# Kernel tuning notes

Measured on AMD Instinct MI355X. Metric: run time of the kernel, lower is better.

Reference implementation:

```python
import jax, jax.numpy as jnp
import numpy as np

H, NH, NKV, HD, I = 4096, 32, 8, 128, 14336
B, S = 1, 2048
THETA = 500000.0
EPS = 1e-5
SCALE = HD ** -0.5


def setup_inputs() -> dict:
    key = jax.random.key(0)
    ks = jax.random.split(key, 8)
    sc = 0.02
    return {
        "positions": jnp.arange(S, dtype=jnp.int32),
        "hidden_states": jax.random.normal(ks[0], (B, S, H), jnp.float32),
        "residual": jax.random.normal(ks[1], (B, S, H), jnp.float32),
        "w_qkv": jax.random.normal(ks[2], ((NH + 2 * NKV) * HD, H), jnp.float32) * sc,
        "w_o": jax.random.normal(ks[3], (H, NH * HD), jnp.float32) * sc,
        "w_gate_up": jax.random.normal(ks[4], (2 * I, H), jnp.float32) * sc,
        "w_down": jax.random.normal(ks[5], (H, I), jnp.float32) * sc,
        "w_ln1": jnp.ones((H,), jnp.float32),
        "w_ln2": jnp.ones((H,), jnp.float32),
    }


def rmsnorm(x, w):
    xf = x.astype(jnp.float32)
    y = xf * jax.lax.rsqrt(jnp.mean(xf * xf, axis=-1, keepdims=True) + EPS)
    return (y * w).astype(x.dtype)


def apply_rope(x, positions):
    # x: [B, S, nh, HD]; neox style: rotate halves
    half = HD // 2
    inv_freq = 1.0 / (THETA ** (jnp.arange(0, half, dtype=jnp.float32) / half))
    freqs = positions.astype(jnp.float32)[:, None] * inv_freq[None, :]  # [S, half]
    cos = jnp.cos(freqs)[None, :, None, :]
    sin = jnp.sin(freqs)[None, :, None, :]
    x1, x2 = x[..., :half], x[..., half:]
    return jnp.concatenate([x1 * cos - x2 * sin, x2 * cos + x1 * sin], axis=-1)


def reference(positions, hidden_states, residual, w_qkv, w_o, w_gate_up, w_down, w_ln1, w_ln2):
    # fused add + RMSNorm (input_layernorm with residual)
    residual = hidden_states + residual
    h = rmsnorm(residual, w_ln1)

    # fused QKV projection
    qkv = jnp.einsum('bsh,oh->bso', h, w_qkv)
    q = qkv[..., : NH * HD].reshape(B, S, NH, HD)
    k = qkv[..., NH * HD: (NH + NKV) * HD].reshape(B, S, NKV, HD)
    v = qkv[..., (NH + NKV) * HD:].reshape(B, S, NKV, HD)

    q = apply_rope(q, positions)
    k = apply_rope(k, positions)

    # GQA: expand kv heads
    rep = NH // NKV
    k = jnp.repeat(k, rep, axis=2)  # [B,S,NH,HD]
    v = jnp.repeat(v, rep, axis=2)

    scores = jnp.einsum('bqhd,bkhd->bhqk', q, k) * SCALE
    causal = jnp.tril(jnp.ones((S, S), bool))
    scores = jnp.where(causal[None, None], scores, jnp.float32(-1e30))
    attn = jax.nn.softmax(scores, axis=-1)
    ctx = jnp.einsum('bhqk,bkhd->bqhd', attn, v).reshape(B, S, NH * HD)
    attn_out = jnp.einsum('bso,ho->bsh', ctx, w_o)

    # fused add + RMSNorm (post_attention_layernorm)
    residual = attn_out + residual
    h = rmsnorm(residual, w_ln2)

    # SwiGLU MLP
    gu = jnp.einsum('bsh,oh->bso', h, w_gate_up)
    gate, up = gu[..., :I], gu[..., I:]
    h = jax.nn.silu(gate) * up
    out = jnp.einsum('bsi,hi->bsh', h, w_down)
    return out, residual
```

## Files before the change

kernel.cpp:

```cpp
#include <hip/hip_runtime.h>

typedef short bf16x8 __attribute__((ext_vector_type(8)));
typedef short short4v __attribute__((ext_vector_type(4)));
typedef float f32x4 __attribute__((ext_vector_type(4)));

#define SCALE_ATTN 0.08838834764831845f

__device__ inline short f2bs(float f) {
    unsigned u = __builtin_bit_cast(unsigned, f);
    unsigned r = (u + 0x7fffu + ((u >> 16) & 1u)) >> 16;
    return (short)(unsigned short)r;
}
__device__ inline float b2f(short s) {
    unsigned u = ((unsigned)(unsigned short)s) << 16;
    return __builtin_bit_cast(float, u);
}
__device__ inline void pack_w(const float4& a, const float4& b, bf16x8& p) {
    p[0] = f2bs(a.x); p[1] = f2bs(a.y); p[2] = f2bs(a.z); p[3] = f2bs(a.w);
    p[4] = f2bs(b.x); p[5] = f2bs(b.y); p[6] = f2bs(b.z); p[7] = f2bs(b.w);
}

__global__ __launch_bounds__(256)
void wconv_kernel(const float* __restrict__ src, short* __restrict__ dst, long n8)
{
    const long stride = (long)gridDim.x << 8;
    for (long i = ((long)blockIdx.x << 8) + threadIdx.x; i < n8; i += stride) {
        const float4 a = ((const float4*)src)[i << 1];
        const float4 b = ((const float4*)src)[(i << 1) + 1];
        bf16x8 p;
        pack_w(a, b, p);
        ((bf16x8*)dst)[i] = p;
    }
}

__global__ __launch_bounds__(256)
void add_rmsnorm_kernel(const float* __restrict__ X, const float* __restrict__ Rin,
                        const float* __restrict__ w, float* __restrict__ Rout,
                        short* __restrict__ Hout)
{
    const int tid = threadIdx.x;
    const long base = (long)blockIdx.x << 12;
    float v[16];
    float ss = 0.f;
#pragma unroll
    for (int p = 0; p < 4; ++p) {
        const int idx = (p << 10) + (tid << 2);
        float4 a = *(const float4*)(X + base + idx);
        if (Rin != nullptr) {
            float4 b = *(const float4*)(Rin + base + idx);
            a.x += b.x; a.y += b.y; a.z += b.z; a.w += b.w;
        }
        v[p*4+0] = a.x; v[p*4+1] = a.y; v[p*4+2] = a.z; v[p*4+3] = a.w;
        ss += a.x*a.x + a.y*a.y + a.z*a.z + a.w*a.w;
    }
#pragma unroll
    for (int dd = 1; dd < 64; dd <<= 1) ss += __shfl_xor(ss, dd);
    __shared__ float red[4];
    if ((tid & 63) == 0) red[tid >> 6] = ss;
    __syncthreads();
    const float tot = red[0] + red[1] + red[2] + red[3];
    const float rstd = rsqrtf(tot * (1.0f / 4096.0f) + 1e-5f);
#pragma unroll
    for (int p = 0; p < 4; ++p) {
        const int idx = (p << 10) + (tid << 2);
        if (Rout != nullptr) {
            float4 b; b.x = v[p*4+0]; b.y = v[p*4+1]; b.z = v[p*4+2]; b.w = v[p*4+3];
            *(float4*)(Rout + base + idx) = b;
        }
        float4 wv4 = *(const float4*)(w + idx);
        short4v hb;
        hb[0] = f2bs(v[p*4+0] * rstd * wv4.x);
        hb[1] = f2bs(v[p*4+1] * rstd * wv4.y);
        hb[2] = f2bs(v[p*4+2] * rstd * wv4.z);
        hb[3] = f2bs(v[p*4+3] * rstd * wv4.w);
        *(short4v*)(Hout + base + idx) = hb;
    }
}

#define BAR()   do { asm volatile("" ::: "memory"); __builtin_amdgcn_s_barrier(); asm volatile("" ::: "memory"); } while (0)
#define LGKM0() asm volatile("s_waitcnt lgkmcnt(0)" ::: "memory")
#define VMW(n)  asm volatile("s_waitcnt vmcnt(" #n ")" ::: "memory")

__device__ inline bf16x8 lds_frag(const short* tile, int row, int kb) {
    const int off = row * 128 + (kb ^ ((row & 7) << 4));
    return *(const bf16x8*)((const char*)tile + off);
}

__device__ inline void stage_half(const short* __restrict__ G, long grow0, long K,
                                  long k0, short* ldsHalf, int wv, int lane)
{
#pragma unroll
    for (int i = 0; i < 2; ++i) {
        short* dst = ldsHalf + ((i << 13) + (wv << 10)) / 2;
        const int off = (wv << 10) + (i << 13) + (lane << 4);
        const int r   = off >> 7;
        const int cb  = off & 127;
        const int gcb = cb ^ ((r & 7) << 4);
        const short* src = G + (grow0 + r) * K + k0 + (gcb >> 1);
        __builtin_amdgcn_global_load_lds(
            (const __attribute__((address_space(1))) void*)(const void*)src,
            (__attribute__((address_space(3))) void*)(void*)dst, 16, 0, 0);
    }
}

#define LOAD_A(T, grp) do {                                        \
    _Pragma("unroll") for (int _m = 0; _m < 4; ++_m) {             \
        const int _row = abase + (grp)*64 + _m*16 + l15;           \
        a[_m][0] = lds_frag(T, _row, l4b);                         \
        a[_m][1] = lds_frag(T, _row, 64 + l4b);                    \
    } } while (0)

#define LOAD_B(T, n0) do {                                         \
    _Pragma("unroll") for (int _n = 0; _n < 2; ++_n) {             \
        const int _row = bbase + ((n0)+_n)*16 + l15;               \
        b[(n0)+_n][0] = lds_frag(T, _row, l4b);                    \
        b[(n0)+_n][1] = lds_frag(T, _row, 64 + l4b);               \
    } } while (0)

#define MFMA16(MB, NB) do {                                                        \
    __builtin_amdgcn_s_setprio(1);                                                 \
    _Pragma("unroll") for (int _m = 0; _m < 4; ++_m)                               \
    _Pragma("unroll") for (int _n = 0; _n < 2; ++_n) {                             \
        acc[(MB)+_m][(NB)+_n] = __builtin_amdgcn_mfma_f32_16x16x32_bf16(           \
            a[_m][0], b[(NB)+_n][0], acc[(MB)+_m][(NB)+_n], 0, 0, 0);              \
        acc[(MB)+_m][(NB)+_n] = __builtin_amdgcn_mfma_f32_16x16x32_bf16(           \
            a[_m][1], b[(NB)+_n][1], acc[(MB)+_m][(NB)+_n], 0, 0, 0);              \
    }                                                                              \
    __builtin_amdgcn_s_setprio(0);                                                 \
} while (0)

template<int EPI>
__global__ __launch_bounds__(512, 2)
void gemm8(const short* __restrict__ A, const short* __restrict__ W,
           float* __restrict__ Cf, short* __restrict__ Cb,
           const float* __restrict__ resid, int N, int K)
{
    __shared__ __align__(16) short As[2][16384];
    __shared__ __align__(16) short Bs[2][16384];

    const int tid  = threadIdx.x;
    const int lane = tid & 63;
    const int wv   = tid >> 6;
    const int wm   = wv >> 2;
    const int wn   = wv & 3;
    const int l15  = lane & 15;
    const int l4b  = (lane >> 4) << 4;

    const int nwg  = gridDim.x << 3;
    const int cpx  = nwg >> 3;
    const int orig = (blockIdx.y * gridDim.x) + blockIdx.x;
    const int lgc  = (orig & 7) * cpx + (orig >> 3);
    const int bx   = lgc >> 3;
    const int by   = lgc & 7;

    const long row0 = (long)by << 8;
    const long col0 = (long)bx << 8;
    const int abase = wm << 7;
    const int bbase = wn << 6;

    f32x4 acc[8][4];
#pragma unroll
    for (int i = 0; i < 8; ++i)
#pragma unroll
        for (int j = 0; j < 4; ++j) acc[i][j] = (f32x4){0.f,0.f,0.f,0.f};

    bf16x8 a[4][2], b[4][2];
    const int iters = K >> 7;

    stage_half(A, row0,       K, 0,  &As[0][0],    wv, lane);
    stage_half(A, row0 + 128, K, 0,  &As[0][8192], wv, lane);
    stage_half(W, col0,       K, 0,  &Bs[0][0],    wv, lane);
    stage_half(W, col0 + 128, K, 0,  &Bs[0][8192], wv, lane);
    stage_half(A, row0,       K, 64, &As[1][0],    wv, lane);
    stage_half(A, row0 + 128, K, 64, &As[1][8192], wv, lane);
    stage_half(W, col0,       K, 64, &Bs[1][0],    wv, lane);
    stage_half(W, col0 + 128, K, 64, &Bs[1][8192], wv, lane);
    VMW(8);
    BAR();

#pragma unroll 1
    for (int it = 0; it < iters; ++it) {
        const long k2 = ((long)(2*it + 2)) << 6;
        const long k3 = k2 + 64;
        const bool pf = (it + 1 < iters);

        LOAD_A(As[0], 0); LOAD_B(Bs[0], 0);
        BAR(); LGKM0(); MFMA16(0, 0); BAR();
        LOAD_B(Bs[0], 2);
        BAR(); LGKM0(); MFMA16(0, 2); BAR();
        LOAD_A(As[0], 1);
        if (pf) stage_half(W, col0, K, k2, &Bs[0][0], wv, lane);
        BAR(); LGKM0(); MFMA16(4, 0); BAR();
        if (pf) {
            stage_half(A, row0,       K, k2, &As[0][0],    wv, lane);
            stage_half(W, col0 + 128, K, k2, &Bs[0][8192], wv, lane);
        }
        VMW(6);
        BAR(); MFMA16(4, 2); BAR();

        LOAD_A(As[1], 0); LOAD_B(Bs[1], 0);
        if (pf) stage_half(A, row0 + 128, K, k2, &As[0][8192], wv, lane);
        BAR(); LGKM0(); MFMA16(0, 0); BAR();
        LOAD_B(Bs[1], 2);
        BAR(); LGKM0(); MFMA16(0, 2); BAR();
        LOAD_A(As[1], 1);
        if (pf) {
            stage_half(W, col0,       K, k3, &Bs[1][0],    wv, lane);
            stage_half(W, col0 + 128, K, k3, &Bs[1][8192], wv, lane);
        }
        BAR(); LGKM0(); MFMA16(4, 0); BAR();
        if (pf) {
            stage_half(A, row0,       K, k3, &As[1][0],    wv, lane);
            stage_half(A, row0 + 128, K, k3, &As[1][8192], wv, lane);
        }
        VMW(8);
        BAR(); MFMA16(4, 2); BAR();
    }

#pragma unroll
    for (int m = 0; m < 8; ++m) {
#pragma unroll
        for (int n = 0; n < 4; ++n) {
            const long gr = row0 + (wm << 7) + m*16 + ((lane >> 4) << 2);
            const long gc = col0 + (wn << 6) + n*16 + l15;
#pragma unroll
            for (int r = 0; r < 4; ++r) {
                const float v = acc[m][n][r];
                const long idx = (gr + r) * N + gc;
                if (EPI == 0)      Cf[idx] = v;
                else if (EPI == 1) Cf[idx] = v + resid[idx];
                else               Cb[idx] = f2bs(v);
            }
        }
    }
}

__global__ __launch_bounds__(128)
void rope_kernel(const int* __restrict__ pos, const float* __restrict__ qkv,
                 short* __restrict__ Qo, short* __restrict__ Ko)
{
    const int h = blockIdx.x;
    const int s = blockIdx.y;
    const int d = threadIdx.x;
    const int j = d & 63;
    const float p = (float)pos[s];
    const float invf = __expf((float)j * -0.20503692895f);
    float sn, cs;
    __sincosf(p * invf, &sn, &cs);
    const long base = (long)s * 6144 + h * 128;
    const float x1 = qkv[base + j];
    const float x2 = qkv[base + 64 + j];
    const float outv = (d < 64) ? (x1 * cs - x2 * sn) : (x2 * cs + x1 * sn);
    const short ob = f2bs(outv);
    if (h < 32) Qo[(long)s * 4096 + h * 128 + d] = ob;
    else        Ko[(long)s * 1024 + (h - 32) * 128 + d] = ob;
}

__global__ __launch_bounds__(256)
void vtrans_kernel(const float* __restrict__ qkv, short* __restrict__ Vt)
{
    __shared__ short tile[64][136];
    const int tid = threadIdx.x;
    const int s0 = blockIdx.x << 6;
    const int h = blockIdx.y;
    {
        const int srow = tid >> 2;
        const int c0 = (tid & 3) << 5;
        const float* src = qkv + (long)(s0 + srow) * 6144 + 5120 + h * 128 + c0;
#pragma unroll
        for (int m = 0; m < 8; ++m) {
            float4 f = *(const float4*)(src + (m << 2));
            tile[srow][c0 + (m << 2) + 0] = f2bs(f.x);
            tile[srow][c0 + (m << 2) + 1] = f2bs(f.y);
            tile[srow][c0 + (m << 2) + 2] = f2bs(f.z);
            tile[srow][c0 + (m << 2) + 3] = f2bs(f.w);
        }
    }
    __syncthreads();
    {
        const int d = tid >> 1;
        const int sc = (tid & 1) << 5;
        short* dst = Vt + ((long)h * 128 + d) * 2048 + s0 + sc;
#pragma unroll
        for (int m = 0; m < 4; ++m) {
            bf16x8 v;
#pragma unroll
            for (int e = 0; e < 8; ++e) v[e] = tile[sc + (m << 3) + e][d];
            *(bf16x8*)(dst + (m << 3)) = v;
        }
    }
}

__global__ __launch_bounds__(256)
void flash_kernel(const short* __restrict__ Qg, const short* __restrict__ Kg,
                  const short* __restrict__ Vtg, short* __restrict__ Ctx)
{
    __shared__ short Qs[64 * 128];
    __shared__ short Ks[64 * 128];
    __shared__ short Vs[128 * 64];
    __shared__ short Ps[4 * 16 * 64];

    const int tid  = threadIdx.x;
    const int lane = tid & 63;
    const int wv   = tid >> 6;
    const int l15  = lane & 15;
    const int l4e  = (lane >> 4) << 3;
    const int qt   = blockIdx.x;
    const int head = blockIdx.y;
    const int q0   = qt << 6;
    const int kvh  = head >> 2;

    {
        const int row = tid >> 2;
        const int c0 = (tid & 3) << 5;
        const short* src = Qg + (long)(q0 + row) * 4096 + head * 128 + c0;
        const int sw = (row & 7) << 3;
#pragma unroll
        for (int m = 0; m < 4; ++m) {
            bf16x8 v = *(const bf16x8*)(src + (m << 3));
            *(bf16x8*)&Qs[row * 128 + ((c0 + (m << 3)) ^ sw)] = v;
        }
    }

    float mrow[4], lrow[4];
    f32x4 o[8];
#pragma unroll
    for (int r = 0; r < 4; ++r) { mrow[r] = -__builtin_inff(); lrow[r] = 0.f; }
#pragma unroll
    for (int d = 0; d < 8; ++d) o[d] = (f32x4){0.f,0.f,0.f,0.f};

    for (int t = 0; t <= qt; ++t) {
        const int kv0 = t << 6;
        __syncthreads();
        {
            const int row = tid >> 2;
            const int c0 = (tid & 3) << 5;
            const short* src = Kg + (long)(kv0 + row) * 1024 + kvh * 128 + c0;
            const int sw = (row & 7) << 3;
#pragma unroll
            for (int m = 0; m < 4; ++m) {
                bf16x8 v = *(const bf16x8*)(src + (m << 3));
                *(bf16x8*)&Ks[row * 128 + ((c0 + (m << 3)) ^ sw)] = v;
            }
        }
        {
            const int d = tid >> 1;
            const int c0 = (tid & 1) << 5;
            const short* src = Vtg + ((long)kvh * 128 + d) * 2048 + kv0 + c0;
            const int sw = (d & 7) << 3;
#pragma unroll
            for (int m = 0; m < 4; ++m) {
                bf16x8 v = *(const bf16x8*)(src + (m << 3));
                *(bf16x8*)&Vs[d * 64 + ((c0 + (m << 3)) ^ sw)] = v;
            }
        }
        __syncthreads();

        bf16x8 qa[4];
        {
            const int qrow = (wv << 4) + l15;
            const int sw = (qrow & 7) << 3;
#pragma unroll
            for (int kk = 0; kk < 4; ++kk)
                qa[kk] = *(const bf16x8*)&Qs[qrow * 128 + ((l4e + (kk << 5)) ^ sw)];
        }
        f32x4 sacc[4];
#pragma unroll
        for (int j = 0; j < 4; ++j) {
            sacc[j] = (f32x4){0.f,0.f,0.f,0.f};
            const int krow = (j << 4) + l15;
            const int sw = (krow & 7) << 3;
#pragma unroll
            for (int kk = 0; kk < 4; ++kk) {
                bf16x8 kb8 = *(const bf16x8*)&Ks[krow * 128 + ((l4e + (kk << 5)) ^ sw)];
                sacc[j] = __builtin_amdgcn_mfma_f32_16x16x32_bf16(qa[kk], kb8, sacc[j], 0, 0, 0);
            }
        }

#pragma unroll
        for (int ri = 0; ri < 4; ++ri) {
            const int grow = q0 + (wv << 4) + ((lane >> 4) << 2) + ri;
            float sv[4];
#pragma unroll
            for (int j = 0; j < 4; ++j) {
                float s = sacc[j][ri] * SCALE_ATTN;
                const int col = kv0 + (j << 4) + l15;
                sv[j] = (col > grow) ? -1e30f : s;
            }
            float mx = fmaxf(fmaxf(sv[0], sv[1]), fmaxf(sv[2], sv[3]));
#pragma unroll
            for (int dd = 1; dd < 16; dd <<= 1) mx = fmaxf(mx, __shfl_xor(mx, dd));
            const float mnew = fmaxf(mrow[ri], mx);
            const float alpha = __expf(mrow[ri] - mnew);
            mrow[ri] = mnew;
            float psum = 0.f;
            short pb[4];
#pragma unroll
            for (int j = 0; j < 4; ++j) {
                float p = __expf(sv[j] - mnew);
                psum += p;
                pb[j] = f2bs(p);
            }
            lrow[ri] = lrow[ri] * alpha + psum;
#pragma unroll
            for (int d = 0; d < 8; ++d) o[d][ri] *= alpha;
            const int prow = ((lane >> 4) << 2) + ri;
            const int sw = (prow & 7) << 3;
#pragma unroll
            for (int j = 0; j < 4; ++j)
                Ps[(wv << 10) + prow * 64 + ((((j << 4) + l15)) ^ sw)] = pb[j];
        }

        bf16x8 pa0, pa1;
        {
            const int prow = l15;
            const int sw = (prow & 7) << 3;
            pa0 = *(const bf16x8*)&Ps[(wv << 10) + prow * 64 + (l4e ^ sw)];
            pa1 = *(const bf16x8*)&Ps[(wv << 10) + prow * 64 + ((l4e + 32) ^ sw)];
        }
#pragma unroll
        for (int fd = 0; fd < 8; ++fd) {
            const int drow = (fd << 4) + l15;
            const int sw = (drow & 7) << 3;
            bf16x8 v0 = *(const bf16x8*)&Vs[drow * 64 + (l4e ^ sw)];
            bf16x8 v1 = *(const bf16x8*)&Vs[drow * 64 + ((l4e + 32) ^ sw)];
            o[fd] = __builtin_amdgcn_mfma_f32_16x16x32_bf16(pa0, v0, o[fd], 0, 0, 0);
            o[fd] = __builtin_amdgcn_mfma_f32_16x16x32_bf16(pa1, v1, o[fd], 0, 0, 0);
        }
    }

    float inv[4];
#pragma unroll
    for (int ri = 0; ri < 4; ++ri) {
        float ls = lrow[ri];
#pragma unroll
        for (int dd = 1; dd < 16; dd <<= 1) ls += __shfl_xor(ls, dd);
        inv[ri] = 1.0f / ls;
    }
#pragma unroll
    for (int fd = 0; fd < 8; ++fd)
#pragma unroll
        for (int ri = 0; ri < 4; ++ri) {
            const long row = q0 + (wv << 4) + ((lane >> 4) << 2) + ri;
            Ctx[row * 4096 + head * 128 + (fd << 4) + l15] = f2bs(o[fd][ri] * inv[ri]);
        }
}

__global__ __launch_bounds__(256)
void silu_kernel(const short* __restrict__ gu, short* __restrict__ hm)
{
    const int s = blockIdx.y;
    const int j = ((blockIdx.x << 8) + threadIdx.x) << 3;
    const short* g = gu + (long)s * 28672 + j;
    bf16x8 gv = *(const bf16x8*)g;
    bf16x8 uv = *(const bf16x8*)(g + 14336);
    bf16x8 ov;
#pragma unroll
    for (int e = 0; e < 8; ++e) {
        const float gf = b2f(gv[e]);
        const float uf = b2f(uv[e]);
        const float r = gf / (1.f + __expf(-gf)) * uf;
        ov[e] = f2bs(r);
    }
    *(bf16x8*)(hm + (long)s * 14336 + j) = ov;
}

extern "C" void kernel_launch(void* const* d_in, const int* in_sizes, int n_in,
                              void* d_out, int out_size, void* d_ws, size_t ws_size,
                              hipStream_t stream)
{
    const int*   positions = (const int*)d_in[0];
    const float* hidden    = (const float*)d_in[1];
    const float* residual  = (const float*)d_in[2];
    const float* w_qkv     = (const float*)d_in[3];
    const float* w_o       = (const float*)d_in[4];
    const float* w_gu      = (const float*)d_in[5];
    const float* w_down    = (const float*)d_in[6];
    const float* w_ln1     = (const float*)d_in[7];
    const float* w_ln2     = (const float*)d_in[8];

    float* out_f   = (float*)d_out;
    float* resid2  = out_f + 8388608;
    float* resid1  = out_f;

    char* wsb = (char*)d_ws;
    short* h1     = (short*)(wsb + 0);
    short* ctx    = (short*)(wsb + 0);
    float* qkvbuf = (float*)(wsb + 16777216);
    short* h2     = (short*)(wsb + 16777216);
    short* qb     = (short*)(wsb + 67108864);
    short* kb     = (short*)(wsb + 83886080);
    short* vt     = (short*)(wsb + 88080384);
    short* gu     = (short*)(wsb + 33554432);
    short* hm     = (short*)(wsb + 150994944);
    short* wbuf   = (short*)(wsb + 209715200);

    add_rmsnorm_kernel<<<2048, 256, 0, stream>>>(hidden, residual, w_ln1, resid1, h1);
    wconv_kernel<<<2048, 256, 0, stream>>>(w_qkv, wbuf, 3145728L);
    gemm8<0><<<dim3(24, 8), 512, 0, stream>>>(h1, wbuf, qkvbuf, nullptr, nullptr, 6144, 4096);
    rope_kernel<<<dim3(40, 2048), 128, 0, stream>>>(positions, qkvbuf, qb, kb);
    vtrans_kernel<<<dim3(32, 8), 256, 0, stream>>>(qkvbuf, vt);
    flash_kernel<<<dim3(32, 32), 256, 0, stream>>>(qb, kb, vt, ctx);
    wconv_kernel<<<2048, 256, 0, stream>>>(w_o, wbuf, 2097152L);
    gemm8<1><<<dim3(16, 8), 512, 0, stream>>>(ctx, wbuf, resid2, nullptr, resid1, 4096, 4096);
    add_rmsnorm_kernel<<<2048, 256, 0, stream>>>(resid2, nullptr, w_ln2, nullptr, h2);
    wconv_kernel<<<2048, 256, 0, stream>>>(w_gu, wbuf, 14680064L);
    gemm8<2><<<dim3(112, 8), 512, 0, stream>>>(h2, wbuf, nullptr, gu, nullptr, 28672, 4096);
    silu_kernel<<<dim3(7, 2048), 256, 0, stream>>>(gu, hm);
    wconv_kernel<<<2048, 256, 0, stream>>>(w_down, wbuf, 7340032L);
    gemm8<0><<<dim3(16, 8), 512, 0, stream>>>(hm, wbuf, out_f, nullptr, nullptr, 4096, 14336);
}
```

Measured before the change: 1.578 ms.

## Add split-K to small-N GEMMs and register double-buffer LDS fragments

Adds a KS template parameter so the O-projection and down-projection GEMMs split K in two across a third grid dimension. This doubles the workgroup count from 128 to 256 so more CUs are busy. The partial sums go to fp32 workspace and are reduced in the following add+rmsnorm kernel or a new add2 kernel. Separately, the GEMM main loop now double-buffers A/B fragments in registers (Aa/Ab, B0/B1) and drops the explicit lgkmcnt waits, so LDS reads overlap with MFMAs. The cost is extra fp32 partial traffic and higher register pressure.

```diff
diff --git a/kernel.cpp b/kernel.cpp
--- a/kernel.cpp
+++ b/kernel.cpp
@@ -34,9 +34,9 @@
 }
 
 __global__ __launch_bounds__(256)
-void add_rmsnorm_kernel(const float* __restrict__ X, const float* __restrict__ Rin,
-                        const float* __restrict__ w, float* __restrict__ Rout,
-                        short* __restrict__ Hout)
+void add_rmsnorm_kernel(const float* __restrict__ X, const float* __restrict__ X2,
+                        const float* __restrict__ Rin, const float* __restrict__ w,
+                        float* __restrict__ Rout, short* __restrict__ Hout)
 {
     const int tid = threadIdx.x;
     const long base = (long)blockIdx.x << 12;
@@ -46,6 +46,10 @@
     for (int p = 0; p < 4; ++p) {
         const int idx = (p << 10) + (tid << 2);
         float4 a = *(const float4*)(X + base + idx);
+        if (X2 != nullptr) {
+            float4 b = *(const float4*)(X2 + base + idx);
+            a.x += b.x; a.y += b.y; a.z += b.z; a.w += b.w;
+        }
         if (Rin != nullptr) {
             float4 b = *(const float4*)(Rin + base + idx);
             a.x += b.x; a.y += b.y; a.z += b.z; a.w += b.w;
@@ -77,8 +81,20 @@
     }
 }
 
+__global__ __launch_bounds__(256)
+void add2_kernel(const float* __restrict__ a, const float* __restrict__ b,
+                 float* __restrict__ o, long n4)
+{
+    const long st = (long)gridDim.x << 8;
+    for (long i = ((long)blockIdx.x << 8) + threadIdx.x; i < n4; i += st) {
+        float4 x = ((const float4*)a)[i];
+        float4 y = ((const float4*)b)[i];
+        x.x += y.x; x.y += y.y; x.z += y.z; x.w += y.w;
+        ((float4*)o)[i] = x;
+    }
+}
+
 #define BAR()   do { asm volatile("" ::: "memory"); __builtin_amdgcn_s_barrier(); asm volatile("" ::: "memory"); } while (0)
-#define LGKM0() asm volatile("s_waitcnt lgkmcnt(0)" ::: "memory")
 #define VMW(n)  asm volatile("s_waitcnt vmcnt(" #n ")" ::: "memory")
 
 __device__ inline bf16x8 lds_frag(const short* tile, int row, int kb) {
@@ -103,33 +119,33 @@
     }
 }
 
-#define LOAD_A(T, grp) do {                                        \
+#define LOADA_(dst, T, grp) do {                                   \
     _Pragma("unroll") for (int _m = 0; _m < 4; ++_m) {             \
         const int _row = abase + (grp)*64 + _m*16 + l15;           \
-        a[_m][0] = lds_frag(T, _row, l4b);                         \
-        a[_m][1] = lds_frag(T, _row, 64 + l4b);                    \
+        dst[_m][0] = lds_frag(T, _row, l4b);                       \
+        dst[_m][1] = lds_frag(T, _row, 64 + l4b);                  \
     } } while (0)
 
-#define LOAD_B(T, n0) do {                                         \
+#define LOADB_(dst, T, n0) do {                                    \
     _Pragma("unroll") for (int _n = 0; _n < 2; ++_n) {             \
         const int _row = bbase + ((n0)+_n)*16 + l15;               \
-        b[(n0)+_n][0] = lds_frag(T, _row, l4b);                    \
-        b[(n0)+_n][1] = lds_frag(T, _row, 64 + l4b);               \
+        dst[_n][0] = lds_frag(T, _row, l4b);                       \
+        dst[_n][1] = lds_frag(T, _row, 64 + l4b);                  \
     } } while (0)
 
-#define MFMA16(MB, NB) do {                                                        \
+#define MFMA16_(AR, BR, MB, NB) do {                                               \
     __builtin_amdgcn_s_setprio(1);                                                 \
     _Pragma("unroll") for (int _m = 0; _m < 4; ++_m)                               \
     _Pragma("unroll") for (int _n = 0; _n < 2; ++_n) {                             \
         acc[(MB)+_m][(NB)+_n] = __builtin_amdgcn_mfma_f32_16x16x32_bf16(           \
-            a[_m][0], b[(NB)+_n][0], acc[(MB)+_m][(NB)+_n], 0, 0, 0);              \
+            AR[_m][0], BR[_n][0], acc[(MB)+_m][(NB)+_n], 0, 0, 0);                 \
         acc[(MB)+_m][(NB)+_n] = __builtin_amdgcn_mfma_f32_16x16x32_bf16(           \
-            a[_m][1], b[(NB)+_n][1], acc[(MB)+_m][(NB)+_n], 0, 0, 0);              \
+            AR[_m][1], BR[_n][1], acc[(MB)+_m][(NB)+_n], 0, 0, 0);                 \
     }                                                                              \
     __builtin_amdgcn_s_setprio(0);                                                 \
 } while (0)
 
-template<int EPI>
+template<int EPI, int KS>
 __global__ __launch_bounds__(512, 2)
 void gemm8(const short* __restrict__ A, const short* __restrict__ W,
            float* __restrict__ Cf, short* __restrict__ Cb,
@@ -146,77 +162,99 @@
     const int l15  = lane & 15;
     const int l4b  = (lane >> 4) << 4;
 
-    const int nwg  = gridDim.x << 3;
+    const int gx   = gridDim.x;
+    const int nwg  = gx * 8 * KS;
     const int cpx  = nwg >> 3;
-    const int orig = (blockIdx.y * gridDim.x) + blockIdx.x;
+    const int orig = (blockIdx.z * 8 + blockIdx.y) * gx + blockIdx.x;
     const int lgc  = (orig & 7) * cpx + (orig >> 3);
-    const int bx   = lgc >> 3;
     const int by   = lgc & 7;
+    const int tq   = lgc >> 3;
+    const int kz   = (KS == 1) ? 0 : (tq % KS);
+    const int bx   = (KS == 1) ? tq : (tq / KS);
 
     const long row0 = (long)by << 8;
     const long col0 = (long)bx << 8;
     const int abase = wm << 7;
     const int bbase = wn << 6;
 
+    const int  Kc    = K / KS;
+    const long kbase = (long)kz * Kc;
+    const int  iters = Kc >> 7;
+
     f32x4 acc[8][4];
 #pragma unroll
     for (int i = 0; i < 8; ++i)
 #pragma unroll
         for (int j = 0; j < 4; ++j) acc[i][j] = (f32x4){0.f,0.f,0.f,0.f};
 
-    bf16x8 a[4][2], b[4][2];
-    const int iters = K >> 7;
-
-    stage_half(A, row0,       K, 0,  &As[0][0],    wv, lane);
-    stage_half(A, row0 + 128, K, 0,  &As[0][8192], wv, lane);
-    stage_half(W, col0,       K, 0,  &Bs[0][0],    wv, lane);
-    stage_half(W, col0 + 128, K, 0,  &Bs[0][8192], wv, lane);
-    stage_half(A, row0,       K, 64, &As[1][0],    wv, lane);
-    stage_half(A, row0 + 128, K, 64, &As[1][8192], wv, lane);
-    stage_half(W, col0,       K, 64, &Bs[1][0],    wv, lane);
-    stage_half(W, col0 + 128, K, 64, &Bs[1][8192], wv, lane);
+    bf16x8 Aa[4][2], Ab[4][2], B0[2][2], B1[2][2];
+
+    stage_half(A, row0,       K, kbase,      &As[0][0],    wv, lane);
+    stage_half(A, row0 + 128, K, kbase,      &As[0][8192], wv, lane);
+    stage_half(W, col0,       K, kbase,      &Bs[0][0],    wv, lane);
+    stage_half(W, col0 + 128, K, kbase,      &Bs[0][8192], wv, lane);
+    stage_half(A, row0,       K, kbase + 64, &As[1][0],    wv, lane);
+    stage_half(A, row0 + 128, K, kbase + 64, &As[1][8192], wv, lane);
+    stage_half(W, col0,       K, kbase + 64, &Bs[1][0],    wv, lane);
+    stage_half(W, col0 + 128, K, kbase + 64, &Bs[1][8192], wv, lane);
     VMW(8);
     BAR();
+    LOADA_(Aa, As[0], 0); LOADB_(B0, Bs[0], 0);
 
 #pragma unroll 1
     for (int it = 0; it < iters; ++it) {
-        const long k2 = ((long)(2*it + 2)) << 6;
+        const long k2 = kbase + ((long)(2*it + 2) << 6);
         const long k3 = k2 + 64;
         const bool pf = (it + 1 < iters);
 
-        LOAD_A(As[0], 0); LOAD_B(Bs[0], 0);
-        BAR(); LGKM0(); MFMA16(0, 0); BAR();
-        LOAD_B(Bs[0], 2);
-        BAR(); LGKM0(); MFMA16(0, 2); BAR();
-        LOAD_A(As[0], 1);
+        BAR();
+        LOADB_(B1, Bs[0], 2);
+        MFMA16_(Aa, B0, 0, 0);
+        BAR();
+        LOADA_(Ab, As[0], 1);
+        MFMA16_(Aa, B1, 0, 2);
+        BAR();
         if (pf) stage_half(W, col0, K, k2, &Bs[0][0], wv, lane);
-        BAR(); LGKM0(); MFMA16(4, 0); BAR();
+        BAR();
+        MFMA16_(Ab, B0, 4, 0);
+        BAR();
         if (pf) {
             stage_half(A, row0,       K, k2, &As[0][0],    wv, lane);
             stage_half(W, col0 + 128, K, k2, &Bs[0][8192], wv, lane);
         }
         VMW(6);
-        BAR(); MFMA16(4, 2); BAR();
-
-        LOAD_A(As[1], 0); LOAD_B(Bs[1], 0);
+        BAR();
+        LOADA_(Aa, As[1], 0); LOADB_(B0, Bs[1], 0);
+        MFMA16_(Ab, B1, 4, 2);
+        BAR();
         if (pf) stage_half(A, row0 + 128, K, k2, &As[0][8192], wv, lane);
-        BAR(); LGKM0(); MFMA16(0, 0); BAR();
-        LOAD_B(Bs[1], 2);
-        BAR(); LGKM0(); MFMA16(0, 2); BAR();
-        LOAD_A(As[1], 1);
+        BAR();
+        LOADB_(B1, Bs[1], 2);
+        MFMA16_(Aa, B0, 0, 0);
+        BAR();
+        LOADA_(Ab, As[1], 1);
+        MFMA16_(Aa, B1, 0, 2);
+        BAR();
         if (pf) {
             stage_half(W, col0,       K, k3, &Bs[1][0],    wv, lane);
             stage_half(W, col0 + 128, K, k3, &Bs[1][8192], wv, lane);
         }
-        BAR(); LGKM0(); MFMA16(4, 0); BAR();
+        BAR();
+        MFMA16_(Ab, B0, 4, 0);
+        BAR();
         if (pf) {
             stage_half(A, row0,       K, k3, &As[1][0],    wv, lane);
             stage_half(A, row0 + 128, K, k3, &As[1][8192], wv, lane);
         }
         VMW(8);
-        BAR(); MFMA16(4, 2); BAR();
-    }
-
+        BAR();
+        if (pf) { LOADA_(Aa, As[0], 0); LOADB_(B0, Bs[0], 0); }
+        MFMA16_(Ab, B1, 4, 2);
+        BAR();
+    }
+
+    float* Cfp = Cf;
+    if (KS > 1) Cfp = Cf + (long)kz * ((long)N << 11);
 #pragma unroll
     for (int m = 0; m < 8; ++m) {
 #pragma unroll
@@ -227,8 +265,8 @@
             for (int r = 0; r < 4; ++r) {
                 const float v = acc[m][n][r];
                 const long idx = (gr + r) * N + gc;
-                if (EPI == 0)      Cf[idx] = v;
-                else if (EPI == 1) Cf[idx] = v + resid[idx];
+                if (EPI == 0)      Cfp[idx] = v;
+                else if (EPI == 1) Cfp[idx] = v + resid[idx];
                 else               Cb[idx] = f2bs(v);
             }
         }
@@ -491,22 +529,25 @@
     short* qb     = (short*)(wsb + 67108864);
     short* kb     = (short*)(wsb + 83886080);
     short* vt     = (short*)(wsb + 88080384);
+    float* Po     = (float*)(wsb + 100663296);
     short* gu     = (short*)(wsb + 33554432);
     short* hm     = (short*)(wsb + 150994944);
+    float* Pd     = (float*)(wsb + 0);
     short* wbuf   = (short*)(wsb + 209715200);
 
-    add_rmsnorm_kernel<<<2048, 256, 0, stream>>>(hidden, residual, w_ln1, resid1, h1);
+    add_rmsnorm_kernel<<<2048, 256, 0, stream>>>(hidden, nullptr, residual, w_ln1, resid1, h1);
     wconv_kernel<<<2048, 256, 0, stream>>>(w_qkv, wbuf, 3145728L);
-    gemm8<0><<<dim3(24, 8), 512, 0, stream>>>(h1, wbuf, qkvbuf, nullptr, nullptr, 6144, 4096);
+    gemm8<0,1><<<dim3(24, 8, 1), 512, 0, stream>>>(h1, wbuf, qkvbuf, nullptr, nullptr, 6144, 4096);
     rope_kernel<<<dim3(40, 2048), 128, 0, stream>>>(positions, qkvbuf, qb, kb);
     vtrans_kernel<<<dim3(32, 8), 256, 0, stream>>>(qkvbuf, vt);
     flash_kernel<<<dim3(32, 32), 256, 0, stream>>>(qb, kb, vt, ctx);
     wconv_kernel<<<2048, 256, 0, stream>>>(w_o, wbuf, 2097152L);
-    gemm8<1><<<dim3(16, 8), 512, 0, stream>>>(ctx, wbuf, resid2, nullptr, resid1, 4096, 4096);
-    add_rmsnorm_kernel<<<2048, 256, 0, stream>>>(resid2, nullptr, w_ln2, nullptr, h2);
+    gemm8<0,2><<<dim3(16, 8, 2), 512, 0, stream>>>(ctx, wbuf, Po, nullptr, nullptr, 4096, 4096);
+    add_rmsnorm_kernel<<<2048, 256, 0, stream>>>(Po, Po + 8388608, resid1, w_ln2, resid2, h2);
     wconv_kernel<<<2048, 256, 0, stream>>>(w_gu, wbuf, 14680064L);
-    gemm8<2><<<dim3(112, 8), 512, 0, stream>>>(h2, wbuf, nullptr, gu, nullptr, 28672, 4096);
+    gemm8<2,1><<<dim3(112, 8, 1), 512, 0, stream>>>(h2, wbuf, nullptr, gu, nullptr, 28672, 4096);
     silu_kernel<<<dim3(7, 2048), 256, 0, stream>>>(gu, hm);
     wconv_kernel<<<2048, 256, 0, stream>>>(w_down, wbuf, 7340032L);
-    gemm8<0><<<dim3(16, 8), 512, 0, stream>>>(hm, wbuf, out_f, nullptr, nullptr, 4096, 14336);
-}
+    gemm8<0,2><<<dim3(16, 8, 2), 512, 0, stream>>>(hm, wbuf, Pd, nullptr, nullptr, 4096, 14336);
+    add2_kernel<<<2048, 256, 0, stream>>>(Pd, Pd + 8388608, out_f, 2097152L);
+}
```

Result: slower. 1.775 ms (+12.5%).

## Split-K for O/down GEMMs and fuse SiLU into gate-up GEMM epilogue

Applied to the files above, without the earlier changes.

Adds a split-K template parameter to the GEMM so the O-projection and down-projection grids run two K-halves into partial buffers. The partials are summed in the following add+RMSNorm kernel and in a new add kernel. The gate/up weights are interleaved in 128-row tiles during conversion so each output tile holds matching gate and up columns. SiLU is then applied in the GEMM epilogue through LDS, which removes the separate SiLU kernel and the bf16 gate-up round trip. The cost is extra partial-sum traffic in fp32 and one more small kernel for the down projection.

```diff
diff --git a/kernel.cpp b/kernel.cpp
--- a/kernel.cpp
+++ b/kernel.cpp
@@ -33,10 +33,25 @@
     }
 }
 
+__global__ __launch_bounds__(512)
+void wconv_gu_kernel(const float* __restrict__ src, short* __restrict__ dst)
+{
+    const int n = blockIdx.x;
+    const int t = n >> 8, r = n & 255;
+    const int orig = (r < 128) ? (t * 128 + r) : (14336 + t * 128 + (r - 128));
+    const float* s = src + (long)orig * 4096;
+    short* d = dst + (long)n * 4096;
+    const int j = threadIdx.x << 3;
+    float4 a = *(const float4*)(s + j);
+    float4 b = *(const float4*)(s + j + 4);
+    bf16x8 p; pack_w(a, b, p);
+    *(bf16x8*)(d + j) = p;
+}
+
 __global__ __launch_bounds__(256)
-void add_rmsnorm_kernel(const float* __restrict__ X, const float* __restrict__ Rin,
-                        const float* __restrict__ w, float* __restrict__ Rout,
-                        short* __restrict__ Hout)
+void add_rmsnorm_kernel(const float* __restrict__ X, const float* __restrict__ X2,
+                        const float* __restrict__ Rin, const float* __restrict__ w,
+                        float* __restrict__ Rout, short* __restrict__ Hout)
 {
     const int tid = threadIdx.x;
     const long base = (long)blockIdx.x << 12;
@@ -46,6 +61,10 @@
     for (int p = 0; p < 4; ++p) {
         const int idx = (p << 10) + (tid << 2);
         float4 a = *(const float4*)(X + base + idx);
+        if (X2 != nullptr) {
+            float4 b = *(const float4*)(X2 + base + idx);
+            a.x += b.x; a.y += b.y; a.z += b.z; a.w += b.w;
+        }
         if (Rin != nullptr) {
             float4 b = *(const float4*)(Rin + base + idx);
             a.x += b.x; a.y += b.y; a.z += b.z; a.w += b.w;
@@ -74,6 +93,19 @@
         hb[2] = f2bs(v[p*4+2] * rstd * wv4.z);
         hb[3] = f2bs(v[p*4+3] * rstd * wv4.w);
         *(short4v*)(Hout + base + idx) = hb;
+    }
+}
+
+__global__ __launch_bounds__(256)
+void add2_kernel(const float* __restrict__ a, const float* __restrict__ b,
+                 float* __restrict__ o, long n4)
+{
+    const long st = (long)gridDim.x << 8;
+    for (long i = ((long)blockIdx.x << 8) + threadIdx.x; i < n4; i += st) {
+        float4 x = ((const float4*)a)[i];
+        float4 y = ((const float4*)b)[i];
+        x.x += y.x; x.y += y.y; x.z += y.z; x.w += y.w;
+        ((float4*)o)[i] = x;
     }
 }
 
@@ -129,11 +161,11 @@
     __builtin_amdgcn_s_setprio(0);                                                 \
 } while (0)
 
-template<int EPI>
+template<int EPI, int KS>
 __global__ __launch_bounds__(512, 2)
 void gemm8(const short* __restrict__ A, const short* __restrict__ W,
            float* __restrict__ Cf, short* __restrict__ Cb,
-           const float* __restrict__ resid, int N, int K)
+           int N, int K)
 {
     __shared__ __align__(16) short As[2][16384];
     __shared__ __align__(16) short Bs[2][16384];
@@ -146,18 +178,25 @@
     const int l15  = lane & 15;
     const int l4b  = (lane >> 4) << 4;
 
-    const int nwg  = gridDim.x << 3;
+    const int gx   = gridDim.x;
+    const int nwg  = gx * 8 * KS;
     const int cpx  = nwg >> 3;
-    const int orig = (blockIdx.y * gridDim.x) + blockIdx.x;
+    const int orig = (blockIdx.z * 8 + blockIdx.y) * gx + blockIdx.x;
     const int lgc  = (orig & 7) * cpx + (orig >> 3);
-    const int bx   = lgc >> 3;
     const int by   = lgc & 7;
+    const int tq   = lgc >> 3;
+    const int kz   = (KS == 1) ? 0 : (tq % KS);
+    const int bx   = (KS == 1) ? tq : (tq / KS);
 
     const long row0 = (long)by << 8;
     const long col0 = (long)bx << 8;
     const int abase = wm << 7;
     const int bbase = wn << 6;
 
+    const int  Kc    = K / KS;
+    const long kbase = (long)kz * Kc;
+    const int  iters = Kc >> 7;
+
     f32x4 acc[8][4];
 #pragma unroll
     for (int i = 0; i < 8; ++i)
@@ -165,22 +204,21 @@
         for (int j = 0; j < 4; ++j) acc[i][j] = (f32x4){0.f,0.f,0.f,0.f};
 
     bf16x8 a[4][2], b[4][2];
-    const int iters = K >> 7;
-
-    stage_half(A, row0,       K, 0,  &As[0][0],    wv, lane);
-    stage_half(A, row0 + 128, K, 0,  &As[0][8192], wv, lane);
-    stage_half(W, col0,       K, 0,  &Bs[0][0],    wv, lane);
-    stage_half(W, col0 + 128, K, 0,  &Bs[0][8192], wv, lane);
-    stage_half(A, row0,       K, 64, &As[1][0],    wv, lane);
-    stage_half(A, row0 + 128, K, 64, &As[1][8192], wv, lane);
-    stage_half(W, col0,       K, 64, &Bs[1][0],    wv, lane);
-    stage_half(W, col0 + 128, K, 64, &Bs[1][8192], wv, lane);
+
+    stage_half(A, row0,       K, kbase,      &As[0][0],    wv, lane);
+    stage_half(A, row0 + 128, K, kbase,      &As[0][8192], wv, lane);
+    stage_half(W, col0,       K, kbase,      &Bs[0][0],    wv, lane);
+    stage_half(W, col0 + 128, K, kbase,      &Bs[0][8192], wv, lane);
+    stage_half(A, row0,       K, kbase + 64, &As[1][0],    wv, lane);
+    stage_half(A, row0 + 128, K, kbase + 64, &As[1][8192], wv, lane);
+    stage_half(W, col0,       K, kbase + 64, &Bs[1][0],    wv, lane);
+    stage_half(W, col0 + 128, K, kbase + 64, &Bs[1][8192], wv, lane);
     VMW(8);
     BAR();
 
 #pragma unroll 1
     for (int it = 0; it < iters; ++it) {
-        const long k2 = ((long)(2*it + 2)) << 6;
+        const long k2 = kbase + ((long)(2*it + 2) << 6);
         const long k3 = k2 + 64;
         const bool pf = (it + 1 < iters);
 
@@ -217,20 +255,43 @@
         BAR(); MFMA16(4, 2); BAR();
     }
 
-#pragma unroll
-    for (int m = 0; m < 8; ++m) {
-#pragma unroll
-        for (int n = 0; n < 4; ++n) {
-            const long gr = row0 + (wm << 7) + m*16 + ((lane >> 4) << 2);
-            const long gc = col0 + (wn << 6) + n*16 + l15;
-#pragma unroll
-            for (int r = 0; r < 4; ++r) {
-                const float v = acc[m][n][r];
-                const long idx = (gr + r) * N + gc;
-                if (EPI == 0)      Cf[idx] = v;
-                else if (EPI == 1) Cf[idx] = v + resid[idx];
-                else               Cb[idx] = f2bs(v);
-            }
+    if (EPI == 0) {
+        float* Cfp = Cf + ((KS > 1) ? (long)kz * ((long)N << 11) : 0);
+#pragma unroll
+        for (int m = 0; m < 8; ++m) {
+#pragma unroll
+            for (int n = 0; n < 4; ++n) {
+                const long gr = row0 + (wm << 7) + m*16 + ((lane >> 4) << 2);
+                const long gc = col0 + (wn << 6) + n*16 + l15;
+#pragma unroll
+                for (int r = 0; r < 4; ++r)
+                    Cfp[(gr + r) * N + gc] = acc[m][n][r];
+            }
+        }
+    } else {
+        float* eps = (float*)&As[0][0];
+        const int r4 = (lane >> 4) << 2;
+        const int rr = tid >> 4;
+        const int cc = (tid & 15) << 3;
+#pragma unroll 1
+        for (int m = 0; m < 8; ++m) {
+            __syncthreads();
+#pragma unroll
+            for (int n = 0; n < 4; ++n)
+#pragma unroll
+                for (int r = 0; r < 4; ++r)
+                    eps[(wm*16 + r4 + r)*272 + (wn << 6) + n*16 + l15] = acc[m][n][r];
+            __syncthreads();
+            const float* rowp = eps + rr * 272;
+            bf16x8 ov;
+#pragma unroll
+            for (int e = 0; e < 8; ++e) {
+                const float g = rowp[cc + e];
+                const float u = rowp[cc + 128 + e];
+                ov[e] = f2bs(g / (1.f + __expf(-g)) * u);
+            }
+            const long grow = row0 + ((rr >> 4) << 7) + m*16 + (rr & 15);
+            *(bf16x8*)(Cb + grow * N + (col0 >> 1) + cc) = ov;
         }
     }
 }
@@ -446,25 +507,6 @@
         }
 }
 
-__global__ __launch_bounds__(256)
-void silu_kernel(const short* __restrict__ gu, short* __restrict__ hm)
-{
-    const int s = blockIdx.y;
-    const int j = ((blockIdx.x << 8) + threadIdx.x) << 3;
-    const short* g = gu + (long)s * 28672 + j;
-    bf16x8 gv = *(const bf16x8*)g;
-    bf16x8 uv = *(const bf16x8*)(g + 14336);
-    bf16x8 ov;
-#pragma unroll
-    for (int e = 0; e < 8; ++e) {
-        const float gf = b2f(gv[e]);
-        const float uf = b2f(uv[e]);
-        const float r = gf / (1.f + __expf(-gf)) * uf;
-        ov[e] = f2bs(r);
-    }
-    *(bf16x8*)(hm + (long)s * 14336 + j) = ov;
-}
-
 extern "C" void kernel_launch(void* const* d_in, const int* in_sizes, int n_in,
                               void* d_out, int out_size, void* d_ws, size_t ws_size,
                               hipStream_t stream)
@@ -491,22 +533,23 @@
     short* qb     = (short*)(wsb + 67108864);
     short* kb     = (short*)(wsb + 83886080);
     short* vt     = (short*)(wsb + 88080384);
-    short* gu     = (short*)(wsb + 33554432);
-    short* hm     = (short*)(wsb + 150994944);
+    short* hm     = (short*)(wsb + 33554432);
+    float* Po     = (float*)(wsb + 100663296);
+    float* Pd     = (float*)(wsb + 100663296);
     short* wbuf   = (short*)(wsb + 209715200);
 
-    add_rmsnorm_kernel<<<2048, 256, 0, stream>>>(hidden, residual, w_ln1, resid1, h1);
+    add_rmsnorm_kernel<<<2048, 256, 0, stream>>>(hidden, nullptr, residual, w_ln1, resid1, h1);
     wconv_kernel<<<2048, 256, 0, stream>>>(w_qkv, wbuf, 3145728L);
-    gemm8<0><<<dim3(24, 8), 512, 0, stream>>>(h1, wbuf, qkvbuf, nullptr, nullptr, 6144, 4096);
+    gemm8<0,1><<<dim3(24, 8, 1), 512, 0, stream>>>(h1, wbuf, qkvbuf, nullptr, 6144, 4096);
     rope_kernel<<<dim3(40, 2048), 128, 0, stream>>>(positions, qkvbuf, qb, kb);
     vtrans_kernel<<<dim3(32, 8), 256, 0, stream>>>(qkvbuf, vt);
     flash_kernel<<<dim3(32, 32), 256, 0, stream>>>(qb, kb, vt, ctx);
     wconv_kernel<<<2048, 256, 0, stream>>>(w_o, wbuf, 2097152L);
-    gemm8<1><<<dim3(16, 8), 512, 0, stream>>>(ctx, wbuf, resid2, nullptr, resid1, 4096, 4096);
-    add_rmsnorm_kernel<<<2048, 256, 0, stream>>>(resid2, nullptr, w_ln2, nullptr, h2);
-    wconv_kernel<<<2048, 256, 0, stream>>>(w_gu, wbuf, 14680064L);
-    gemm8<2><<<dim3(112, 8), 512, 0, stream>>>(h2, wbuf, nullptr, gu, nullptr, 28672, 4096);
-    silu_kernel<<<dim3(7, 2048), 256, 0, stream>>>(gu, hm);
+    gemm8<0,2><<<dim3(16, 8, 2), 512, 0, stream>>>(ctx, wbuf, Po, nullptr, 4096, 4096);
+    add_rmsnorm_kernel<<<2048, 256, 0, stream>>>(Po, Po + 8388608, resid1, w_ln2, resid2, h2);
+    wconv_gu_kernel<<<28672, 512, 0, stream>>>(w_gu, wbuf);
+    gemm8<3,1><<<dim3(112, 8, 1), 512, 0, stream>>>(h2, wbuf, nullptr, hm, 14336, 4096);
     wconv_kernel<<<2048, 256, 0, stream>>>(w_down, wbuf, 7340032L);
-    gemm8<0><<<dim3(16, 8), 512, 0, stream>>>(hm, wbuf, out_f, nullptr, nullptr, 4096, 14336);
-}
+    gemm8<0,2><<<dim3(16, 8, 2), 512, 0, stream>>>(hm, wbuf, Pd, nullptr, 4096, 14336);
+    add2_kernel<<<2048, 256, 0, stream>>>(Pd, Pd + 8388608, out_f, 2097152L);
+}
```

Result: faster. 1.462 ms (-7.3%).
